# Kernel optimization log

Measured on AMD Instinct MI355X. Metric: run time of the kernel, lower is better.

Reference implementation:

```python
import jax, jax.numpy as jnp
import numpy as np

B, S, D = 4, 2048, 1024
H, DK, DV = 16, 64, 64

def setup_inputs() -> dict:
    key = jax.random.key(0)
    ks = jax.random.split(key, 14)
    sc = 0.02
    return {
        "q": jax.random.normal(ks[0], (B, S, D), jnp.float32),
        "k": jax.random.normal(ks[1], (B, S, D), jnp.float32),
        "v": jax.random.normal(ks[2], (B, S, D), jnp.float32),
        "Wq": jax.random.normal(ks[3], (D, H * DK), jnp.float32) * sc,
        "bq": jnp.zeros((H * DK,), jnp.float32),
        "Wk": jax.random.normal(ks[4], (D, H * DK), jnp.float32) * sc,
        "bk": jnp.zeros((H * DK,), jnp.float32),
        "Wv": jax.random.normal(ks[5], (D, H * DV), jnp.float32) * sc,
        "bv": jnp.zeros((H * DV,), jnp.float32),
        "Wo": jax.random.normal(ks[6], (H * DV, D), jnp.float32) * sc,
        "bo": jnp.zeros((D,), jnp.float32),
        "gamma": jnp.ones((D,), jnp.float32),
        "beta": jnp.zeros((D,), jnp.float32),
    }

def _layer_norm(x, gamma, beta, eps=1e-5):
    mu = jnp.mean(x, axis=-1, keepdims=True)
    var = jnp.mean(jnp.square(x - mu), axis=-1, keepdims=True)
    return (x - mu) * jax.lax.rsqrt(var + eps) * gamma + beta

def reference(q, k, v, Wq, bq, Wk, bk, Wv, bv, Wo, bo, gamma, beta):
    b, lq, _ = q.shape
    lk = k.shape[1]
    # projections -> [b, h, len, d]
    Q = (q @ Wq + bq).reshape(b, lq, H, DK).transpose(0, 2, 1, 3)
    K = (k @ Wk + bk).reshape(b, lk, H, DK).transpose(0, 2, 1, 3)
    V = (v @ Wv + bv).reshape(b, lk, H, DV).transpose(0, 2, 1, 3)
    scores = jnp.einsum("bhqd,bhkd->bhqk", Q, K) / np.sqrt(DK).astype(np.float32)
    attn = jax.nn.softmax(scores, axis=-1)
    out = jnp.einsum("bhqk,bhkd->bhqd", attn, V)
    out = out.transpose(0, 2, 1, 3).reshape(b, lq, H * DV)
    out = out @ Wo + bo
    # dropout is identity in eval mode
    out = _layer_norm(out + q, gamma, beta)
    return (out, attn)
```

## Files before the change

### kernel.cpp

```cpp
#include <hip/hip_runtime.h>
#include <stdint.h>

typedef unsigned short u16;
typedef unsigned int   u32;
typedef __attribute__((ext_vector_type(8))) short bf16x8;
typedef __attribute__((ext_vector_type(4))) float f32x4;
typedef __attribute__((ext_vector_type(4))) u32   u32x4;
typedef __attribute__((ext_vector_type(2))) u32   u32x2;

#define BB 4
#define SS 2048
#define DD 1024
#define HH 16
#define QSCALE 0.18033688011112042f

__device__ __forceinline__ u16 f2b(float f){
  u32 u = __builtin_bit_cast(u32, f);
  u32 r = (u + 0x7FFFu + ((u >> 16) & 1u)) >> 16;
  return (u16)r;
}
__device__ __forceinline__ float b2f(u16 h){
  return __builtin_bit_cast(float, (u32)h << 16);
}
__device__ __forceinline__ u32 cvtpk(float lo, float hi){
  u32 r; asm("v_cvt_pk_bf16_f32 %0, %1, %2" : "=v"(r) : "v"(lo), "v"(hi)); return r;
}

__device__ __forceinline__ void gload16(const u16* g, u16* l){
  __builtin_amdgcn_global_load_lds(
      (const __attribute__((address_space(1))) void*)(uintptr_t)g,
      (__attribute__((address_space(3))) void*)(uintptr_t)l,
      16, 0, 0);
}

__global__ __launch_bounds__(256)
void cvt_bf16_3(const float* __restrict__ q, const float* __restrict__ k,
                const float* __restrict__ v, u16* __restrict__ qo,
                u16* __restrict__ ko, u16* __restrict__ vo, int npack)
{
  const float* in = blockIdx.y == 0 ? q : (blockIdx.y == 1 ? k : v);
  u16* out        = blockIdx.y == 0 ? qo : (blockIdx.y == 1 ? ko : vo);
  for(int i = blockIdx.x * 256 + threadIdx.x; i < npack; i += gridDim.x * 256){
    const float4* p = (const float4*)in + 2 * (size_t)i;
    float4 a = p[0], b = p[1];
    u32x4 o;
    o.x = f2b(a.x) | ((u32)f2b(a.y) << 16);
    o.y = f2b(a.z) | ((u32)f2b(a.w) << 16);
    o.z = f2b(b.x) | ((u32)f2b(b.y) << 16);
    o.w = f2b(b.z) | ((u32)f2b(b.w) << 16);
    ((u32x4*)out)[i] = o;
  }
}

__global__ __launch_bounds__(256)
void transpose_cvt4(const float* __restrict__ W0, const float* __restrict__ W1,
                    const float* __restrict__ W2, const float* __restrict__ W3,
                    u16* __restrict__ T0, u16* __restrict__ T1,
                    u16* __restrict__ T2, u16* __restrict__ T3)
{
  const float* W = blockIdx.z == 0 ? W0 : (blockIdx.z == 1 ? W1 : (blockIdx.z == 2 ? W2 : W3));
  u16*        Wt = blockIdx.z == 0 ? T0 : (blockIdx.z == 1 ? T1 : (blockIdx.z == 2 ? T2 : T3));
  __shared__ float tile[64][65];
  const int tid = threadIdx.x;
  const int n0 = blockIdx.x * 64, k0 = blockIdx.y * 64;
  const int lr = tid >> 4, lc = tid & 15;
  #pragma unroll
  for(int i = 0; i < 4; ++i){
    float4 v = *(const float4*)(W + (size_t)(k0 + lr + 16*i) * DD + n0 + lc * 4);
    tile[lr + 16*i][lc*4 + 0] = v.x;
    tile[lr + 16*i][lc*4 + 1] = v.y;
    tile[lr + 16*i][lc*4 + 2] = v.z;
    tile[lr + 16*i][lc*4 + 3] = v.w;
  }
  __syncthreads();
  #pragma unroll
  for(int j = 0; j < 2; ++j){
    int idx = j * 256 + tid;
    int row = idx >> 3, seg = idx & 7;
    u32x4 o;
    o.x = f2b(tile[seg*8+0][row]) | ((u32)f2b(tile[seg*8+1][row]) << 16);
    o.y = f2b(tile[seg*8+2][row]) | ((u32)f2b(tile[seg*8+3][row]) << 16);
    o.z = f2b(tile[seg*8+4][row]) | ((u32)f2b(tile[seg*8+5][row]) << 16);
    o.w = f2b(tile[seg*8+6][row]) | ((u32)f2b(tile[seg*8+7][row]) << 16);
    *(u32x4*)(Wt + (size_t)(n0 + row) * DD + k0 + seg * 8) = o;
  }
}

__global__ __launch_bounds__(256)
void gemm_qkv(const u16* __restrict__ qA, const u16* __restrict__ kA, const u16* __restrict__ vA,
              const u16* __restrict__ BtQ, const u16* __restrict__ BtK, const u16* __restrict__ BtV,
              const float* __restrict__ bq, const float* __restrict__ bk, const float* __restrict__ bv,
              u16* __restrict__ Qo, u16* __restrict__ Ko, u16* __restrict__ Vo)
{
  const int mode = blockIdx.z;
  const u16* A   = mode == 0 ? qA  : (mode == 1 ? kA  : vA);
  const u16* Bt  = mode == 0 ? BtQ : (mode == 1 ? BtK : BtV);
  const float* bias = mode == 0 ? bq : (mode == 1 ? bk : bv);
  u16* Cout      = mode == 0 ? Qo  : (mode == 1 ? Ko  : Vo);

  __shared__ __align__(16) u16 smem[16384];
  u16* As = smem;
  u16* Bs = smem + 128*32;
  const int tid = threadIdx.x;
  const int w = tid >> 6, ln = tid & 63, g = ln >> 4, c16 = ln & 15;
  const int m0 = blockIdx.y * 128, n0 = blockIdx.x * 128;
  const int wr = (w >> 1) * 64, wc = (w & 1) * 64;

  f32x4 acc[4][4] = {};

  for(int kt = 0; kt < 1024; kt += 32){
    __syncthreads();
    {
      const int f0 = w * 2;
      #pragma unroll
      for(int j = 0; j < 2; ++j){
        int e = ((f0 + j) * 64 + ln) * 8;
        gload16(Bt + (size_t)(n0 + (e >> 5)) * 1024 + kt + (e & 31),
                Bs + (size_t)(f0 + j) * 512);
        gload16(A + (size_t)(m0 + (e >> 5)) * 1024 + kt + (e & 31),
                As + (size_t)(f0 + j) * 512);
      }
    }
    __syncthreads();
    bf16x8 a[4], b[4];
    #pragma unroll
    for(int mi = 0; mi < 4; ++mi)
      a[mi] = *(const bf16x8*)(As + (wr + mi*16 + c16) * 32 + g * 8);
    #pragma unroll
    for(int ni = 0; ni < 4; ++ni)
      b[ni] = *(const bf16x8*)(Bs + (wc + ni*16 + c16) * 32 + g * 8);
    #pragma unroll
    for(int mi = 0; mi < 4; ++mi)
      #pragma unroll
      for(int ni = 0; ni < 4; ++ni)
        acc[mi][ni] = __builtin_amdgcn_mfma_f32_16x16x32_bf16(a[mi], b[ni], acc[mi][ni], 0, 0, 0);
  }
  __syncthreads();

  char* st = (char*)smem + w * 8192;
  const float sc = (mode == 0) ? QSCALE : 1.f;
  const int bb = m0 >> 11;
  const int h  = (n0 + wc) >> 6;
  const int sbase = (m0 + wr) & 2047;

  if(mode < 2){
    #pragma unroll
    for(int ni = 0; ni < 4; ++ni){
      const float bvv = bias[n0 + wc + ni*16 + c16];
      const int gr = ni*2 + (c16 >> 3);
      const int within = (c16 & 7) * 2;
      #pragma unroll
      for(int mi = 0; mi < 4; ++mi)
        #pragma unroll
        for(int e = 0; e < 4; ++e){
          const int row = mi*16 + g*4 + e;
          *(u16*)(st + row*128 + ((gr ^ (row & 7)) << 4) + within)
              = f2b((acc[mi][ni][e] + bvv) * sc);
        }
    }
    asm volatile("s_waitcnt lgkmcnt(0)" ::: "memory");
    const int r8 = ln >> 3, jl = ln & 7;
    #pragma unroll
    for(int ii = 0; ii < 8; ++ii){
      const int row = ii*8 + r8;
      u16* dst = Cout + (((size_t)(bb*HH + h) * SS) + sbase + row) * 64 + jl*8;
      *(u32x4*)dst = *(const u32x4*)(st + row*128 + ((jl ^ (row & 7)) << 4));
    }
  } else {
    #pragma unroll
    for(int ni = 0; ni < 4; ++ni){
      const float bvv = bias[n0 + wc + ni*16 + c16];
      const int row = ni*16 + c16;
      #pragma unroll
      for(int mi = 0; mi < 4; ++mi)
        #pragma unroll
        for(int e = 0; e < 4; ++e){
          const int sl = mi*16 + g*4 + e;
          const int gr = sl >> 3;
          *(u16*)(st + row*128 + ((gr ^ (row & 7)) << 4) + (sl & 7) * 2)
              = f2b(acc[mi][ni][e] + bvv);
        }
    }
    asm volatile("s_waitcnt lgkmcnt(0)" ::: "memory");
    const int r8 = ln >> 3, jl = ln & 7;
    #pragma unroll
    for(int ii = 0; ii < 8; ++ii){
      const int d = ii*8 + r8;
      u16* dst = Cout + ((size_t)(bb*HH + h) * 64 + (n0 + wc - ((n0+wc)>>6<<6)) + d) * SS + sbase + jl*8;
      *(u32x4*)dst = *(const u32x4*)(st + d*128 + ((jl ^ (d & 7)) << 4));
    }
  }
}

__global__ __launch_bounds__(256)
void gemm_o(const u16* __restrict__ A, const u16* __restrict__ Bt,
            const float* __restrict__ bias, u16* __restrict__ Cout)
{
  __shared__ __align__(16) u16 smem[16384];
  u16* As = smem;
  u16* Bs = smem + 128*32;
  const int tid = threadIdx.x;
  const int w = tid >> 6, ln = tid & 63, g = ln >> 4, c16 = ln & 15;
  const int m0 = blockIdx.y * 128, n0 = blockIdx.x * 128;
  const int wr = (w >> 1) * 64, wc = (w & 1) * 64;

  f32x4 acc[4][4] = {};

  for(int kt = 0; kt < 1024; kt += 32){
    __syncthreads();
    {
      const int f0 = w * 2;
      #pragma unroll
      for(int j = 0; j < 2; ++j){
        int e = ((f0 + j) * 64 + ln) * 8;
        gload16(Bt + (size_t)(n0 + (e >> 5)) * 1024 + kt + (e & 31),
                Bs + (size_t)(f0 + j) * 512);
        gload16(A + (size_t)(m0 + (e >> 5)) * 1024 + kt + (e & 31),
                As + (size_t)(f0 + j) * 512);
      }
    }
    __syncthreads();
    bf16x8 a[4], b[4];
    #pragma unroll
    for(int mi = 0; mi < 4; ++mi)
      a[mi] = *(const bf16x8*)(As + (wr + mi*16 + c16) * 32 + g * 8);
    #pragma unroll
    for(int ni = 0; ni < 4; ++ni)
      b[ni] = *(const bf16x8*)(Bs + (wc + ni*16 + c16) * 32 + g * 8);
    #pragma unroll
    for(int mi = 0; mi < 4; ++mi)
      #pragma unroll
      for(int ni = 0; ni < 4; ++ni)
        acc[mi][ni] = __builtin_amdgcn_mfma_f32_16x16x32_bf16(a[mi], b[ni], acc[mi][ni], 0, 0, 0);
  }
  __syncthreads();

  char* st = (char*)smem + w * 8192;
  #pragma unroll
  for(int ni = 0; ni < 4; ++ni){
    const float bvv = bias[n0 + wc + ni*16 + c16];
    const int gr = ni*2 + (c16 >> 3);
    const int within = (c16 & 7) * 2;
    #pragma unroll
    for(int mi = 0; mi < 4; ++mi)
      #pragma unroll
      for(int e = 0; e < 4; ++e){
        const int row = mi*16 + g*4 + e;
        *(u16*)(st + row*128 + ((gr ^ (row & 7)) << 4) + within)
            = f2b(acc[mi][ni][e] + bvv);
      }
  }
  asm volatile("s_waitcnt lgkmcnt(0)" ::: "memory");
  const int r8 = ln >> 3, jl = ln & 7;
  #pragma unroll
  for(int ii = 0; ii < 8; ++ii){
    const int row = ii*8 + r8;
    u16* dst = Cout + (size_t)(m0 + wr + row) * 1024 + n0 + wc + jl*8;
    *(u32x4*)dst = *(const u32x4*)(st + row*128 + ((jl ^ (row & 7)) << 4));
  }
}

__global__ __launch_bounds__(256)
void attn8(const u16* __restrict__ Qb, const u16* __restrict__ Kb,
           const u16* __restrict__ Vt, float* __restrict__ attn_out,
           u16* __restrict__ AO)
{
  __shared__ __align__(16) u16 shm[32768];
  const int tid = threadIdx.x, w = tid >> 6, ln = tid & 63, g = ln >> 4, c = ln & 15;
  const int bh = blockIdx.y;
  const int q0 = blockIdx.x * 128 + w * 32;

  const u16* Qp = Qb + ((size_t)bh * SS + q0) * 64;
  const u16* Kp = Kb + (size_t)bh * SS * 64;
  const u16* Vp = Vt + (size_t)bh * 64 * SS;

  const bf16x8 bq00 = *(const bf16x8*)(Qp + c * 64 + g * 8);
  const bf16x8 bq01 = *(const bf16x8*)(Qp + c * 64 + 32 + g * 8);
  const bf16x8 bq10 = *(const bf16x8*)(Qp + (16 + c) * 64 + g * 8);
  const bf16x8 bq11 = *(const bf16x8*)(Qp + (16 + c) * 64 + 32 + g * 8);

  auto stageK = [&](int slot, int t){
    const u16* src = Kp + (size_t)t * 64 * 64;
    #pragma unroll
    for(int j = 0; j < 2; ++j){
      int idx = j * 256 + tid;
      int r = idx >> 3, s5 = idx & 7;
      gload16(src + r * 64 + (((s5 ^ (r & 7))) << 3), shm + slot * 4096 + (idx << 3));
    }
  };
  auto stageV = [&](int slot, int t){
    #pragma unroll
    for(int j = 0; j < 2; ++j){
      int idx = j * 256 + tid;
      int r = idx >> 3, s5 = idx & 7;
      gload16(Vp + (size_t)r * SS + t * 64 + (((s5 ^ (r & 7))) << 3),
              shm + 12288 + slot * 4096 + (idx << 3));
    }
  };

  float l0 = 0.f, l1 = 0.f;
  auto comp1 = [&](const u16* kb_){
    f32x4 s[2][4] = {};
    #pragma unroll
    for(int ch = 0; ch < 4; ++ch){
      const int r = ch * 16 + c;
      bf16x8 ka0 = *(const bf16x8*)(kb_ + r * 64 + ((g       ^ (c & 7)) << 3));
      bf16x8 ka1 = *(const bf16x8*)(kb_ + r * 64 + (((4 + g) ^ (c & 7)) << 3));
      s[0][ch] = __builtin_amdgcn_mfma_f32_16x16x32_bf16(ka0, bq00, s[0][ch], 0, 0, 0);
      s[0][ch] = __builtin_amdgcn_mfma_f32_16x16x32_bf16(ka1, bq01, s[0][ch], 0, 0, 0);
      s[1][ch] = __builtin_amdgcn_mfma_f32_16x16x32_bf16(ka0, bq10, s[1][ch], 0, 0, 0);
      s[1][ch] = __builtin_amdgcn_mfma_f32_16x16x32_bf16(ka1, bq11, s[1][ch], 0, 0, 0);
    }
    #pragma unroll
    for(int ch = 0; ch < 4; ++ch)
      #pragma unroll
      for(int e = 0; e < 4; ++e){
        l0 += __builtin_amdgcn_exp2f(s[0][ch][e]);
        l1 += __builtin_amdgcn_exp2f(s[1][ch][e]);
      }
  };

  stageK(0, 0); stageK(1, 1);
  asm volatile("s_waitcnt vmcnt(2)" ::: "memory");
  __builtin_amdgcn_s_barrier();
  for(int t = 0; t < 32; t += 2){
    if(t < 30){ stageK((t + 2) & 3, t + 2); stageK((t + 3) & 3, t + 3); }
    __builtin_amdgcn_sched_barrier(0);
    comp1(shm + (t & 3) * 4096);
    if(t < 30) asm volatile("s_waitcnt vmcnt(4)" ::: "memory");
    else       asm volatile("s_waitcnt vmcnt(0)" ::: "memory");
    __builtin_amdgcn_sched_barrier(0);
    comp1(shm + ((t + 1) & 3) * 4096);
    if(t < 30) asm volatile("s_waitcnt vmcnt(2)" ::: "memory");
    __builtin_amdgcn_s_barrier();
  }
  l0 += __shfl_xor(l0, 16, 64); l0 += __shfl_xor(l0, 32, 64);
  l1 += __shfl_xor(l1, 16, 64); l1 += __shfl_xor(l1, 32, 64);
  const float rl0 = 1.f / l0, rl1 = 1.f / l1;

  f32x4 acc[2][4] = {};
  float* aout = attn_out + ((size_t)bh * SS + q0) * SS;
  u16* pw0 = shm + 24576 + w * 2048;
  u16* pw1 = pw0 + 1024;

  stageK(0, 0); stageV(0, 0); stageK(1, 1); stageV(1, 1);
  asm volatile("s_waitcnt vmcnt(4)" ::: "memory");
  __builtin_amdgcn_s_barrier();

  for(int t = 0; t < 32; ++t){
    if(t < 30){ stageK((t + 2) % 3, t + 2); stageV((t + 2) % 3, t + 2); }
    __builtin_amdgcn_sched_barrier(0);
    const int kv0 = t * 64;
    const u16* kb_ = shm + (t % 3) * 4096;
    const u16* vb_ = shm + 12288 + (t % 3) * 4096;

    f32x4 s[2][4] = {};
    __builtin_amdgcn_s_setprio(1);
    #pragma unroll
    for(int ch = 0; ch < 4; ++ch){
      const int r = ch * 16 + c;
      bf16x8 ka0 = *(const bf16x8*)(kb_ + r * 64 + ((g       ^ (c & 7)) << 3));
      bf16x8 ka1 = *(const bf16x8*)(kb_ + r * 64 + (((4 + g) ^ (c & 7)) << 3));
      s[0][ch] = __builtin_amdgcn_mfma_f32_16x16x32_bf16(ka0, bq00, s[0][ch], 0, 0, 0);
      s[0][ch] = __builtin_amdgcn_mfma_f32_16x16x32_bf16(ka1, bq01, s[0][ch], 0, 0, 0);
      s[1][ch] = __builtin_amdgcn_mfma_f32_16x16x32_bf16(ka0, bq10, s[1][ch], 0, 0, 0);
      s[1][ch] = __builtin_amdgcn_mfma_f32_16x16x32_bf16(ka1, bq11, s[1][ch], 0, 0, 0);
    }
    __builtin_amdgcn_s_setprio(0);

    #pragma unroll
    for(int qb = 0; qb < 2; ++qb){
      const float rl = qb ? rl1 : rl0;
      u16* pw = qb ? pw1 : pw0;
      #pragma unroll
      for(int ch = 0; ch < 4; ++ch){
        float p0 = __builtin_amdgcn_exp2f(s[qb][ch][0]) * rl;
        float p1 = __builtin_amdgcn_exp2f(s[qb][ch][1]) * rl;
        float p2 = __builtin_amdgcn_exp2f(s[qb][ch][2]) * rl;
        float p3 = __builtin_amdgcn_exp2f(s[qb][ch][3]) * rl;
        u32x2 pk2 = { cvtpk(p0, p1), cvtpk(p2, p3) };
        *(u32x2*)((char*)pw + c * 128 + (((ch * 2 + (g >> 1)) ^ (c & 7)) << 4) + ((g & 1) << 3)) = pk2;
      }
    }
    asm volatile("s_waitcnt lgkmcnt(0)" ::: "memory");
    __builtin_amdgcn_sched_barrier(0);

    __builtin_amdgcn_s_setprio(1);
    #pragma unroll
    for(int kc = 0; kc < 2; ++kc){
      bf16x8 ap0 = *(const bf16x8*)((const char*)pw0 + c * 128 + (((kc * 4 + g) ^ (c & 7)) << 4));
      bf16x8 ap1 = *(const bf16x8*)((const char*)pw1 + c * 128 + (((kc * 4 + g) ^ (c & 7)) << 4));
      #pragma unroll
      for(int ni = 0; ni < 4; ++ni){
        bf16x8 bv = *(const bf16x8*)(vb_ + (ni * 16 + c) * 64 + (((kc * 4 + g) ^ (c & 7)) << 3));
        acc[0][ni] = __builtin_amdgcn_mfma_f32_16x16x32_bf16(ap0, bv, acc[0][ni], 0, 0, 0);
        acc[1][ni] = __builtin_amdgcn_mfma_f32_16x16x32_bf16(ap1, bv, acc[1][ni], 0, 0, 0);
      }
    }
    __builtin_amdgcn_s_setprio(0);

    {
      const int r8 = ln >> 3;
      const int jl = ln & 7;
      #pragma unroll
      for(int qb = 0; qb < 2; ++qb){
        const u16* pw = qb ? pw1 : pw0;
        #pragma unroll
        for(int rh = 0; rh < 2; ++rh){
          const int r = rh * 8 + r8;
          #pragma unroll
          for(int chf = 0; chf < 2; ++chf){
            const int jg = chf * 8 + jl;
            const int ch2 = jg >> 2, g2 = jg & 3;
            const int slot = ch2 * 2 + (g2 >> 1);
            u32x2 pk = *(const u32x2*)((const char*)pw + r * 128 +
                         (((slot ^ (r & 7))) << 4) + ((g2 & 1) << 3));
            f32x4 o;
            o[0] = b2f((u16)(pk.x & 0xFFFFu)); o[1] = b2f((u16)(pk.x >> 16));
            o[2] = b2f((u16)(pk.y & 0xFFFFu)); o[3] = b2f((u16)(pk.y >> 16));
            *(f32x4*)(aout + (size_t)(qb * 16 + r) * SS + kv0 + jg * 4) = o;
          }
        }
      }
    }

    if(t == 0)       asm volatile("s_waitcnt vmcnt(12)" ::: "memory");
    else if(t < 30)  asm volatile("s_waitcnt vmcnt(20)" ::: "memory");
    else if(t == 30) asm volatile("s_waitcnt vmcnt(16)" ::: "memory");
    __builtin_amdgcn_s_barrier();
  }

  u16* aos = pw0;
  #pragma unroll
  for(int qb = 0; qb < 2; ++qb)
    #pragma unroll
    for(int ni = 0; ni < 4; ++ni)
      #pragma unroll
      for(int e = 0; e < 4; ++e)
        aos[(qb * 16 + 4 * g + e) * 64 + ni * 16 + c] = f2b(acc[qb][ni][e]);
  asm volatile("s_waitcnt lgkmcnt(0)" ::: "memory");
  __builtin_amdgcn_sched_barrier(0);
  {
    const int bb = bh >> 4, h = bh & 15;
    #pragma unroll
    for(int p2 = 0; p2 < 4; ++p2){
      int idx = p2 * 64 + ln;
      int row = idx >> 3, col16 = (idx & 7) * 8;
      u16* dst = AO + ((size_t)bb * SS + q0 + row) * 1024 + h * 64 + col16;
      *(u32x4*)dst = *(const u32x4*)(aos + row * 64 + col16);
    }
  }
}

__global__ __launch_bounds__(256)
void ln_kernel(const u16* __restrict__ tmpb, const float* __restrict__ qin,
               const float* __restrict__ gamma, const float* __restrict__ beta,
               float* __restrict__ out)
{
  __shared__ float rs[4], rs2[4];
  const int row = blockIdx.x, tid = threadIdx.x;
  const int w = tid >> 6, ln = tid & 63;
  const uint2 tv = *(const uint2*)(tmpb + (size_t)row * 1024 + tid * 4);
  const float4 q4 = *(const float4*)(qin + (size_t)row * 1024 + tid * 4);
  const float xs0 = b2f((u16)(tv.x & 0xFFFFu)) + q4.x;
  const float xs1 = b2f((u16)(tv.x >> 16))     + q4.y;
  const float xs2 = b2f((u16)(tv.y & 0xFFFFu)) + q4.z;
  const float xs3 = b2f((u16)(tv.y >> 16))     + q4.w;
  float s  = xs0 + xs1 + xs2 + xs3;
  float s2 = xs0*xs0 + xs1*xs1 + xs2*xs2 + xs3*xs3;
  #pragma unroll
  for(int m = 1; m < 64; m <<= 1){
    s  += __shfl_xor(s,  m, 64);
    s2 += __shfl_xor(s2, m, 64);
  }
  if(ln == 0){ rs[w] = s; rs2[w] = s2; }
  __syncthreads();
  s  = rs[0]  + rs[1]  + rs[2]  + rs[3];
  s2 = rs2[0] + rs2[1] + rs2[2] + rs2[3];
  const float mu   = s * (1.f / 1024.f);
  const float var  = s2 * (1.f / 1024.f) - mu * mu;
  const float rstd = rsqrtf(var + 1e-5f);
  const float4 g4 = *(const float4*)(gamma + tid * 4);
  const float4 b4 = *(const float4*)(beta + tid * 4);
  float4 o;
  o.x = (xs0 - mu) * rstd * g4.x + b4.x;
  o.y = (xs1 - mu) * rstd * g4.y + b4.y;
  o.z = (xs2 - mu) * rstd * g4.z + b4.z;
  o.w = (xs3 - mu) * rstd * g4.w + b4.w;
  *(float4*)(out + (size_t)row * 1024 + tid * 4) = o;
}

extern "C" void kernel_launch(void* const* d_in, const int* in_sizes, int n_in,
                              void* d_out, int out_size, void* d_ws, size_t ws_size,
                              hipStream_t stream)
{
  (void)in_sizes; (void)n_in; (void)out_size; (void)ws_size;
  const float* q     = (const float*)d_in[0];
  const float* k     = (const float*)d_in[1];
  const float* v     = (const float*)d_in[2];
  const float* Wq    = (const float*)d_in[3];
  const float* bq    = (const float*)d_in[4];
  const float* Wk    = (const float*)d_in[5];
  const float* bk    = (const float*)d_in[6];
  const float* Wv    = (const float*)d_in[7];
  const float* bv    = (const float*)d_in[8];
  const float* Wo    = (const float*)d_in[9];
  const float* bo    = (const float*)d_in[10];
  const float* gamma = (const float*)d_in[11];
  const float* beta  = (const float*)d_in[12];

  char* p = (char*)d_ws;
  auto alloc = [&](size_t bytes) -> void* {
    void* r = (void*)p; p += (bytes + 255) & ~(size_t)255; return r;
  };
  const size_t NTOK = (size_t)BB * SS;
  u16* WtQ  = (u16*)alloc((size_t)DD * DD * 2);
  u16* WtK  = (u16*)alloc((size_t)DD * DD * 2);
  u16* WtV  = (u16*)alloc((size_t)DD * DD * 2);
  u16* WtO  = (u16*)alloc((size_t)DD * DD * 2);
  u16* Qb   = (u16*)alloc(NTOK * DD * 2);
  u16* Kb   = (u16*)alloc(NTOK * DD * 2);
  u16* Vtb  = (u16*)alloc(NTOK * DD * 2);
  u16* AO   = (u16*)alloc(NTOK * DD * 2);
  u16* qbf  = (u16*)alloc(NTOK * DD * 2);
  u16* kbf  = (u16*)alloc(NTOK * DD * 2);
  u16* vbf  = (u16*)alloc(NTOK * DD * 2);
  u16* tmpb = (u16*)alloc(NTOK * DD * 2);

  float* out0 = (float*)d_out;
  float* attn = out0 + NTOK * DD;

  const int NPACK = (int)(NTOK * DD / 8);
  cvt_bf16_3<<<dim3(1024, 3), 256, 0, stream>>>(q, k, v, qbf, kbf, vbf, NPACK);

  transpose_cvt4<<<dim3(16, 16, 4), 256, 0, stream>>>(
      Wq, Wk, Wv, Wo, WtQ, WtK, WtV, WtO);

  gemm_qkv<<<dim3(8, 64, 3), 256, 0, stream>>>(
      qbf, kbf, vbf, WtQ, WtK, WtV, bq, bk, bv, Qb, Kb, Vtb);

  attn8<<<dim3(16, 64), 256, 0, stream>>>(Qb, Kb, Vtb, attn, AO);

  gemm_o<<<dim3(8, 64), 256, 0, stream>>>(AO, WtO, bo, tmpb);
  ln_kernel<<<dim3(8192), 256, 0, stream>>>(tmpb, q, gamma, beta, out0);
}
```

Before: 461.6 us.

## Process two query tiles per block, fusing tile B's row-sum pass into tile A's output pass

Each attention block now handles two 128-row query groups. The softmax denominator pass for the second group is folded into the probability/PV pass of the first group, so K is streamed three times per two groups instead of four. The grid is also reordered so blockIdx.x indexes batch-head. This cuts K reloads and the separate sum pass for half the work, at the cost of fewer blocks (512 vs 1024), more registers for the extra Q fragments, and longer serial work per block.

```diff
diff --git a/kernel.cpp b/kernel.cpp
--- a/kernel.cpp
+++ b/kernel.cpp
@@ -260,24 +260,43 @@
   }
 }
 
+#define QKT(KB, Q00, Q01, Q10, Q11, S) do{                                             \
+  _Pragma("unroll")                                                                    \
+  for(int ch_ = 0; ch_ < 4; ++ch_){                                                    \
+    const int r_ = ch_ * 16 + c;                                                       \
+    bf16x8 ka0_ = *(const bf16x8*)((KB) + r_ * 64 + ((g       ^ (c & 7)) << 3));       \
+    bf16x8 ka1_ = *(const bf16x8*)((KB) + r_ * 64 + (((4 + g) ^ (c & 7)) << 3));       \
+    S[0][ch_] = __builtin_amdgcn_mfma_f32_16x16x32_bf16(ka0_, Q00, S[0][ch_], 0,0,0);  \
+    S[0][ch_] = __builtin_amdgcn_mfma_f32_16x16x32_bf16(ka1_, Q01, S[0][ch_], 0,0,0);  \
+    S[1][ch_] = __builtin_amdgcn_mfma_f32_16x16x32_bf16(ka0_, Q10, S[1][ch_], 0,0,0);  \
+    S[1][ch_] = __builtin_amdgcn_mfma_f32_16x16x32_bf16(ka1_, Q11, S[1][ch_], 0,0,0);  \
+  }                                                                                    \
+}while(0)
+
 __global__ __launch_bounds__(256)
-void attn8(const u16* __restrict__ Qb, const u16* __restrict__ Kb,
+void attn9(const u16* __restrict__ Qb, const u16* __restrict__ Kb,
            const u16* __restrict__ Vt, float* __restrict__ attn_out,
            u16* __restrict__ AO)
 {
   __shared__ __align__(16) u16 shm[32768];
   const int tid = threadIdx.x, w = tid >> 6, ln = tid & 63, g = ln >> 4, c = ln & 15;
-  const int bh = blockIdx.y;
-  const int q0 = blockIdx.x * 128 + w * 32;
-
-  const u16* Qp = Qb + ((size_t)bh * SS + q0) * 64;
-  const u16* Kp = Kb + (size_t)bh * SS * 64;
-  const u16* Vp = Vt + (size_t)bh * 64 * SS;
-
-  const bf16x8 bq00 = *(const bf16x8*)(Qp + c * 64 + g * 8);
-  const bf16x8 bq01 = *(const bf16x8*)(Qp + c * 64 + 32 + g * 8);
-  const bf16x8 bq10 = *(const bf16x8*)(Qp + (16 + c) * 64 + g * 8);
-  const bf16x8 bq11 = *(const bf16x8*)(Qp + (16 + c) * 64 + 32 + g * 8);
+  const int bh = blockIdx.x;
+  const int q0A = blockIdx.y * 256 + w * 32;
+  const int q0B = q0A + 128;
+
+  const u16* QpA = Qb + ((size_t)bh * SS + q0A) * 64;
+  const u16* QpB = Qb + ((size_t)bh * SS + q0B) * 64;
+  const u16* Kp  = Kb + (size_t)bh * SS * 64;
+  const u16* Vp  = Vt + (size_t)bh * 64 * SS;
+
+  const bf16x8 qA00 = *(const bf16x8*)(QpA + c * 64 + g * 8);
+  const bf16x8 qA01 = *(const bf16x8*)(QpA + c * 64 + 32 + g * 8);
+  const bf16x8 qA10 = *(const bf16x8*)(QpA + (16 + c) * 64 + g * 8);
+  const bf16x8 qA11 = *(const bf16x8*)(QpA + (16 + c) * 64 + 32 + g * 8);
+  const bf16x8 qB00 = *(const bf16x8*)(QpB + c * 64 + g * 8);
+  const bf16x8 qB01 = *(const bf16x8*)(QpB + c * 64 + 32 + g * 8);
+  const bf16x8 qB10 = *(const bf16x8*)(QpB + (16 + c) * 64 + g * 8);
+  const bf16x8 qB11 = *(const bf16x8*)(QpB + (16 + c) * 64 + 32 + g * 8);
 
   auto stageK = [&](int slot, int t){
     const u16* src = Kp + (size_t)t * 64 * 64;
@@ -298,75 +317,32 @@
     }
   };
 
-  float l0 = 0.f, l1 = 0.f;
-  auto comp1 = [&](const u16* kb_){
-    f32x4 s[2][4] = {};
-    #pragma unroll
-    for(int ch = 0; ch < 4; ++ch){
-      const int r = ch * 16 + c;
-      bf16x8 ka0 = *(const bf16x8*)(kb_ + r * 64 + ((g       ^ (c & 7)) << 3));
-      bf16x8 ka1 = *(const bf16x8*)(kb_ + r * 64 + (((4 + g) ^ (c & 7)) << 3));
-      s[0][ch] = __builtin_amdgcn_mfma_f32_16x16x32_bf16(ka0, bq00, s[0][ch], 0, 0, 0);
-      s[0][ch] = __builtin_amdgcn_mfma_f32_16x16x32_bf16(ka1, bq01, s[0][ch], 0, 0, 0);
-      s[1][ch] = __builtin_amdgcn_mfma_f32_16x16x32_bf16(ka0, bq10, s[1][ch], 0, 0, 0);
-      s[1][ch] = __builtin_amdgcn_mfma_f32_16x16x32_bf16(ka1, bq11, s[1][ch], 0, 0, 0);
-    }
-    #pragma unroll
-    for(int ch = 0; ch < 4; ++ch)
-      #pragma unroll
-      for(int e = 0; e < 4; ++e){
-        l0 += __builtin_amdgcn_exp2f(s[0][ch][e]);
-        l1 += __builtin_amdgcn_exp2f(s[1][ch][e]);
-      }
-  };
-
-  stageK(0, 0); stageK(1, 1);
-  asm volatile("s_waitcnt vmcnt(2)" ::: "memory");
-  __builtin_amdgcn_s_barrier();
-  for(int t = 0; t < 32; t += 2){
-    if(t < 30){ stageK((t + 2) & 3, t + 2); stageK((t + 3) & 3, t + 3); }
-    __builtin_amdgcn_sched_barrier(0);
-    comp1(shm + (t & 3) * 4096);
-    if(t < 30) asm volatile("s_waitcnt vmcnt(4)" ::: "memory");
-    else       asm volatile("s_waitcnt vmcnt(0)" ::: "memory");
-    __builtin_amdgcn_sched_barrier(0);
-    comp1(shm + ((t + 1) & 3) * 4096);
-    if(t < 30) asm volatile("s_waitcnt vmcnt(2)" ::: "memory");
-    __builtin_amdgcn_s_barrier();
-  }
-  l0 += __shfl_xor(l0, 16, 64); l0 += __shfl_xor(l0, 32, 64);
-  l1 += __shfl_xor(l1, 16, 64); l1 += __shfl_xor(l1, 32, 64);
-  const float rl0 = 1.f / l0, rl1 = 1.f / l1;
-
-  f32x4 acc[2][4] = {};
-  float* aout = attn_out + ((size_t)bh * SS + q0) * SS;
   u16* pw0 = shm + 24576 + w * 2048;
   u16* pw1 = pw0 + 1024;
 
-  stageK(0, 0); stageV(0, 0); stageK(1, 1); stageV(1, 1);
-  asm volatile("s_waitcnt vmcnt(4)" ::: "memory");
-  __builtin_amdgcn_s_barrier();
-
-  for(int t = 0; t < 32; ++t){
-    if(t < 30){ stageK((t + 2) % 3, t + 2); stageV((t + 2) % 3, t + 2); }
-    __builtin_amdgcn_sched_barrier(0);
+  auto p2_tile = [&](int t, const u16* kb_, const u16* vb_,
+                     const bf16x8& Q00, const bf16x8& Q01, const bf16x8& Q10, const bf16x8& Q11,
+                     float rl0, float rl1, f32x4 (&acc)[2][4], float* aout, bool withB,
+                     float& lB0, float& lB1){
     const int kv0 = t * 64;
-    const u16* kb_ = shm + (t % 3) * 4096;
-    const u16* vb_ = shm + 12288 + (t % 3) * 4096;
-
     f32x4 s[2][4] = {};
     __builtin_amdgcn_s_setprio(1);
-    #pragma unroll
-    for(int ch = 0; ch < 4; ++ch){
-      const int r = ch * 16 + c;
-      bf16x8 ka0 = *(const bf16x8*)(kb_ + r * 64 + ((g       ^ (c & 7)) << 3));
-      bf16x8 ka1 = *(const bf16x8*)(kb_ + r * 64 + (((4 + g) ^ (c & 7)) << 3));
-      s[0][ch] = __builtin_amdgcn_mfma_f32_16x16x32_bf16(ka0, bq00, s[0][ch], 0, 0, 0);
-      s[0][ch] = __builtin_amdgcn_mfma_f32_16x16x32_bf16(ka1, bq01, s[0][ch], 0, 0, 0);
-      s[1][ch] = __builtin_amdgcn_mfma_f32_16x16x32_bf16(ka0, bq10, s[1][ch], 0, 0, 0);
-      s[1][ch] = __builtin_amdgcn_mfma_f32_16x16x32_bf16(ka1, bq11, s[1][ch], 0, 0, 0);
-    }
+    QKT(kb_, Q00, Q01, Q10, Q11, s);
     __builtin_amdgcn_s_setprio(0);
+
+    if(withB){
+      f32x4 sb[2][4] = {};
+      __builtin_amdgcn_s_setprio(1);
+      QKT(kb_, qB00, qB01, qB10, qB11, sb);
+      __builtin_amdgcn_s_setprio(0);
+      #pragma unroll
+      for(int ch = 0; ch < 4; ++ch)
+        #pragma unroll
+        for(int e = 0; e < 4; ++e){
+          lB0 += __builtin_amdgcn_exp2f(sb[0][ch][e]);
+          lB1 += __builtin_amdgcn_exp2f(sb[1][ch][e]);
+        }
+    }
 
     #pragma unroll
     for(int qb = 0; qb < 2; ++qb){
@@ -428,19 +404,19 @@
     else if(t < 30)  asm volatile("s_waitcnt vmcnt(20)" ::: "memory");
     else if(t == 30) asm volatile("s_waitcnt vmcnt(16)" ::: "memory");
     __builtin_amdgcn_s_barrier();
-  }
-
-  u16* aos = pw0;
-  #pragma unroll
-  for(int qb = 0; qb < 2; ++qb)
-    #pragma unroll
-    for(int ni = 0; ni < 4; ++ni)
-      #pragma unroll
-      for(int e = 0; e < 4; ++e)
-        aos[(qb * 16 + 4 * g + e) * 64 + ni * 16 + c] = f2b(acc[qb][ni][e]);
-  asm volatile("s_waitcnt lgkmcnt(0)" ::: "memory");
-  __builtin_amdgcn_sched_barrier(0);
-  {
+  };
+
+  auto ao_epilogue = [&](f32x4 (&acc)[2][4], int q0){
+    u16* aos = pw0;
+    #pragma unroll
+    for(int qb = 0; qb < 2; ++qb)
+      #pragma unroll
+      for(int ni = 0; ni < 4; ++ni)
+        #pragma unroll
+        for(int e = 0; e < 4; ++e)
+          aos[(qb * 16 + 4 * g + e) * 64 + ni * 16 + c] = f2b(acc[qb][ni][e]);
+    asm volatile("s_waitcnt lgkmcnt(0)" ::: "memory");
+    __builtin_amdgcn_sched_barrier(0);
     const int bb = bh >> 4, h = bh & 15;
     #pragma unroll
     for(int p2 = 0; p2 < 4; ++p2){
@@ -449,7 +425,72 @@
       u16* dst = AO + ((size_t)bb * SS + q0 + row) * 1024 + h * 64 + col16;
       *(u32x4*)dst = *(const u32x4*)(aos + row * 64 + col16);
     }
-  }
+  };
+
+  float l0 = 0.f, l1 = 0.f;
+  auto comp1 = [&](const u16* kb_){
+    f32x4 s[2][4] = {};
+    QKT(kb_, qA00, qA01, qA10, qA11, s);
+    #pragma unroll
+    for(int ch = 0; ch < 4; ++ch)
+      #pragma unroll
+      for(int e = 0; e < 4; ++e){
+        l0 += __builtin_amdgcn_exp2f(s[0][ch][e]);
+        l1 += __builtin_amdgcn_exp2f(s[1][ch][e]);
+      }
+  };
+
+  stageK(0, 0); stageK(1, 1);
+  asm volatile("s_waitcnt vmcnt(2)" ::: "memory");
+  __builtin_amdgcn_s_barrier();
+  for(int t = 0; t < 32; t += 2){
+    if(t < 30){ stageK((t + 2) & 3, t + 2); stageK((t + 3) & 3, t + 3); }
+    __builtin_amdgcn_sched_barrier(0);
+    comp1(shm + (t & 3) * 4096);
+    if(t < 30) asm volatile("s_waitcnt vmcnt(4)" ::: "memory");
+    else       asm volatile("s_waitcnt vmcnt(0)" ::: "memory");
+    __builtin_amdgcn_sched_barrier(0);
+    comp1(shm + ((t + 1) & 3) * 4096);
+    if(t < 30) asm volatile("s_waitcnt vmcnt(2)" ::: "memory");
+    __builtin_amdgcn_s_barrier();
+  }
+  l0 += __shfl_xor(l0, 16, 64); l0 += __shfl_xor(l0, 32, 64);
+  l1 += __shfl_xor(l1, 16, 64); l1 += __shfl_xor(l1, 32, 64);
+  const float rlA0 = 1.f / l0, rlA1 = 1.f / l1;
+
+  f32x4 accA[2][4] = {};
+  float lB0 = 0.f, lB1 = 0.f;
+  float* aoutA = attn_out + ((size_t)bh * SS + q0A) * SS;
+
+  stageK(0, 0); stageV(0, 0); stageK(1, 1); stageV(1, 1);
+  asm volatile("s_waitcnt vmcnt(4)" ::: "memory");
+  __builtin_amdgcn_s_barrier();
+  for(int t = 0; t < 32; ++t){
+    if(t < 30){ stageK((t + 2) % 3, t + 2); stageV((t + 2) % 3, t + 2); }
+    __builtin_amdgcn_sched_barrier(0);
+    p2_tile(t, shm + (t % 3) * 4096, shm + 12288 + (t % 3) * 4096,
+            qA00, qA01, qA10, qA11, rlA0, rlA1, accA, aoutA, true, lB0, lB1);
+  }
+  ao_epilogue(accA, q0A);
+
+  lB0 += __shfl_xor(lB0, 16, 64); lB0 += __shfl_xor(lB0, 32, 64);
+  lB1 += __shfl_xor(lB1, 16, 64); lB1 += __shfl_xor(lB1, 32, 64);
+  const float rlB0 = 1.f / lB0, rlB1 = 1.f / lB1;
+
+  f32x4 accB[2][4] = {};
+  float dum0, dum1;
+  float* aoutB = attn_out + ((size_t)bh * SS + q0B) * SS;
+
+  stageK(0, 0); stageV(0, 0); stageK(1, 1); stageV(1, 1);
+  asm volatile("s_waitcnt vmcnt(4)" ::: "memory");
+  __builtin_amdgcn_s_barrier();
+  for(int t = 0; t < 32; ++t){
+    if(t < 30){ stageK((t + 2) % 3, t + 2); stageV((t + 2) % 3, t + 2); }
+    __builtin_amdgcn_sched_barrier(0);
+    p2_tile(t, shm + (t % 3) * 4096, shm + 12288 + (t % 3) * 4096,
+            qB00, qB01, qB10, qB11, rlB0, rlB1, accB, aoutB, false, dum0, dum1);
+  }
+  ao_epilogue(accB, q0B);
 }
 
 __global__ __launch_bounds__(256)
@@ -539,7 +580,7 @@
   gemm_qkv<<<dim3(8, 64, 3), 256, 0, stream>>>(
       qbf, kbf, vbf, WtQ, WtK, WtV, bq, bk, bv, Qb, Kb, Vtb);
 
-  attn8<<<dim3(16, 64), 256, 0, stream>>>(Qb, Kb, Vtb, attn, AO);
+  attn9<<<dim3(64, 8), 256, 0, stream>>>(Qb, Kb, Vtb, attn, AO);
 
   gemm_o<<<dim3(8, 64), 256, 0, stream>>>(AO, WtO, bo, tmpb);
   ln_kernel<<<dim3(8192), 256, 0, stream>>>(tmpb, q, gamma, beta, out0);
```

After: 536.7 us. +16.3%, slower.

## Double GEMM K-tile to 64 with XOR-swizzled LDS; one-wave-per-row LayerNorm

Applied to the files above, without the earlier changes.

The shared GEMM main loop now stages a K-step of 64 instead of 32. Global loads are placed into LDS with an XOR swizzle so the MFMA operand reads avoid bank conflicts. This halves the number of barrier-separated iterations in the QKV and output projections while keeping the same LDS footprint. The LayerNorm kernel now gives each wave a full row with a shuffle-only reduction, removing the shared-memory reduction and block barrier, at the cost of more registers per thread.

```diff
diff --git a/kernel.cpp b/kernel.cpp
--- a/kernel.cpp
+++ b/kernel.cpp
@@ -86,6 +86,48 @@
   }
 }
 
+#define GEMM_CORE(A_, Bt_)                                                             \
+  f32x4 acc[4][4] = {};                                                                \
+  for(int kt = 0; kt < 1024; kt += 64){                                                \
+    __syncthreads();                                                                   \
+    {                                                                                  \
+      const int f0 = w * 4;                                                            \
+      _Pragma("unroll")                                                                \
+      for(int j = 0; j < 4; ++j){                                                      \
+        int idx = (f0 + j) * 64 + ln;                                                  \
+        int row = idx >> 3, s5 = idx & 7;                                              \
+        int gcol = (s5 ^ (row & 7)) * 8;                                               \
+        gload16(Bt_ + (size_t)(n0 + row) * 1024 + kt + gcol, Bs + (size_t)(f0+j)*512); \
+        gload16(A_  + (size_t)(m0 + row) * 1024 + kt + gcol, As + (size_t)(f0+j)*512); \
+      }                                                                                \
+    }                                                                                  \
+    __syncthreads();                                                                   \
+    bf16x8 a0[4], a1[4], b0[4], b1[4];                                                 \
+    _Pragma("unroll")                                                                  \
+    for(int mi = 0; mi < 4; ++mi){                                                     \
+      const int r = wr + mi*16 + c16;                                                  \
+      a0[mi] = *(const bf16x8*)(As + r * 64 + ((g       ^ (r & 7)) << 3));             \
+      a1[mi] = *(const bf16x8*)(As + r * 64 + (((4 + g) ^ (r & 7)) << 3));             \
+    }                                                                                  \
+    _Pragma("unroll")                                                                  \
+    for(int ni = 0; ni < 4; ++ni){                                                     \
+      const int r = wc + ni*16 + c16;                                                  \
+      b0[ni] = *(const bf16x8*)(Bs + r * 64 + ((g       ^ (r & 7)) << 3));             \
+      b1[ni] = *(const bf16x8*)(Bs + r * 64 + (((4 + g) ^ (r & 7)) << 3));             \
+    }                                                                                  \
+    _Pragma("unroll")                                                                  \
+    for(int mi = 0; mi < 4; ++mi)                                                      \
+      _Pragma("unroll")                                                                \
+      for(int ni = 0; ni < 4; ++ni)                                                    \
+        acc[mi][ni] = __builtin_amdgcn_mfma_f32_16x16x32_bf16(a0[mi], b0[ni], acc[mi][ni], 0, 0, 0); \
+    _Pragma("unroll")                                                                  \
+    for(int mi = 0; mi < 4; ++mi)                                                      \
+      _Pragma("unroll")                                                                \
+      for(int ni = 0; ni < 4; ++ni)                                                    \
+        acc[mi][ni] = __builtin_amdgcn_mfma_f32_16x16x32_bf16(a1[mi], b1[ni], acc[mi][ni], 0, 0, 0); \
+  }                                                                                    \
+  __syncthreads();
+
 __global__ __launch_bounds__(256)
 void gemm_qkv(const u16* __restrict__ qA, const u16* __restrict__ kA, const u16* __restrict__ vA,
               const u16* __restrict__ BtQ, const u16* __restrict__ BtK, const u16* __restrict__ BtV,
@@ -100,42 +142,13 @@
 
   __shared__ __align__(16) u16 smem[16384];
   u16* As = smem;
-  u16* Bs = smem + 128*32;
+  u16* Bs = smem + 128*64;
   const int tid = threadIdx.x;
   const int w = tid >> 6, ln = tid & 63, g = ln >> 4, c16 = ln & 15;
   const int m0 = blockIdx.y * 128, n0 = blockIdx.x * 128;
   const int wr = (w >> 1) * 64, wc = (w & 1) * 64;
 
-  f32x4 acc[4][4] = {};
-
-  for(int kt = 0; kt < 1024; kt += 32){
-    __syncthreads();
-    {
-      const int f0 = w * 2;
-      #pragma unroll
-      for(int j = 0; j < 2; ++j){
-        int e = ((f0 + j) * 64 + ln) * 8;
-        gload16(Bt + (size_t)(n0 + (e >> 5)) * 1024 + kt + (e & 31),
-                Bs + (size_t)(f0 + j) * 512);
-        gload16(A + (size_t)(m0 + (e >> 5)) * 1024 + kt + (e & 31),
-                As + (size_t)(f0 + j) * 512);
-      }
-    }
-    __syncthreads();
-    bf16x8 a[4], b[4];
-    #pragma unroll
-    for(int mi = 0; mi < 4; ++mi)
-      a[mi] = *(const bf16x8*)(As + (wr + mi*16 + c16) * 32 + g * 8);
-    #pragma unroll
-    for(int ni = 0; ni < 4; ++ni)
-      b[ni] = *(const bf16x8*)(Bs + (wc + ni*16 + c16) * 32 + g * 8);
-    #pragma unroll
-    for(int mi = 0; mi < 4; ++mi)
-      #pragma unroll
-      for(int ni = 0; ni < 4; ++ni)
-        acc[mi][ni] = __builtin_amdgcn_mfma_f32_16x16x32_bf16(a[mi], b[ni], acc[mi][ni], 0, 0, 0);
-  }
-  __syncthreads();
+  GEMM_CORE(A, Bt)
 
   char* st = (char*)smem + w * 8192;
   const float sc = (mode == 0) ? QSCALE : 1.f;
@@ -198,42 +211,13 @@
 {
   __shared__ __align__(16) u16 smem[16384];
   u16* As = smem;
-  u16* Bs = smem + 128*32;
+  u16* Bs = smem + 128*64;
   const int tid = threadIdx.x;
   const int w = tid >> 6, ln = tid & 63, g = ln >> 4, c16 = ln & 15;
   const int m0 = blockIdx.y * 128, n0 = blockIdx.x * 128;
   const int wr = (w >> 1) * 64, wc = (w & 1) * 64;
 
-  f32x4 acc[4][4] = {};
-
-  for(int kt = 0; kt < 1024; kt += 32){
-    __syncthreads();
-    {
-      const int f0 = w * 2;
-      #pragma unroll
-      for(int j = 0; j < 2; ++j){
-        int e = ((f0 + j) * 64 + ln) * 8;
-        gload16(Bt + (size_t)(n0 + (e >> 5)) * 1024 + kt + (e & 31),
-                Bs + (size_t)(f0 + j) * 512);
-        gload16(A + (size_t)(m0 + (e >> 5)) * 1024 + kt + (e & 31),
-                As + (size_t)(f0 + j) * 512);
-      }
-    }
-    __syncthreads();
-    bf16x8 a[4], b[4];
-    #pragma unroll
-    for(int mi = 0; mi < 4; ++mi)
-      a[mi] = *(const bf16x8*)(As + (wr + mi*16 + c16) * 32 + g * 8);
-    #pragma unroll
-    for(int ni = 0; ni < 4; ++ni)
-      b[ni] = *(const bf16x8*)(Bs + (wc + ni*16 + c16) * 32 + g * 8);
-    #pragma unroll
-    for(int mi = 0; mi < 4; ++mi)
-      #pragma unroll
-      for(int ni = 0; ni < 4; ++ni)
-        acc[mi][ni] = __builtin_amdgcn_mfma_f32_16x16x32_bf16(a[mi], b[ni], acc[mi][ni], 0, 0, 0);
-  }
-  __syncthreads();
+  GEMM_CORE(A, Bt)
 
   char* st = (char*)smem + w * 8192;
   #pragma unroll
@@ -457,37 +441,45 @@
                const float* __restrict__ gamma, const float* __restrict__ beta,
                float* __restrict__ out)
 {
-  __shared__ float rs[4], rs2[4];
-  const int row = blockIdx.x, tid = threadIdx.x;
-  const int w = tid >> 6, ln = tid & 63;
-  const uint2 tv = *(const uint2*)(tmpb + (size_t)row * 1024 + tid * 4);
-  const float4 q4 = *(const float4*)(qin + (size_t)row * 1024 + tid * 4);
-  const float xs0 = b2f((u16)(tv.x & 0xFFFFu)) + q4.x;
-  const float xs1 = b2f((u16)(tv.x >> 16))     + q4.y;
-  const float xs2 = b2f((u16)(tv.y & 0xFFFFu)) + q4.z;
-  const float xs3 = b2f((u16)(tv.y >> 16))     + q4.w;
-  float s  = xs0 + xs1 + xs2 + xs3;
-  float s2 = xs0*xs0 + xs1*xs1 + xs2*xs2 + xs3*xs3;
+  const int tid = threadIdx.x, w = tid >> 6, ln = tid & 63;
+  const int row = blockIdx.x * 4 + w;
+  const u16*   tp = tmpb + (size_t)row * 1024;
+  const float* qp = qin  + (size_t)row * 1024;
+  float xs[16];
+  float s = 0.f, s2 = 0.f;
+  #pragma unroll
+  for(int ck = 0; ck < 4; ++ck){
+    const int col = ck * 256 + ln * 4;
+    const uint2 tv = *(const uint2*)(tp + col);
+    const float4 q4 = *(const float4*)(qp + col);
+    float x0 = b2f((u16)(tv.x & 0xFFFFu)) + q4.x;
+    float x1 = b2f((u16)(tv.x >> 16))     + q4.y;
+    float x2 = b2f((u16)(tv.y & 0xFFFFu)) + q4.z;
+    float x3 = b2f((u16)(tv.y >> 16))     + q4.w;
+    xs[ck*4+0] = x0; xs[ck*4+1] = x1; xs[ck*4+2] = x2; xs[ck*4+3] = x3;
+    s  += x0 + x1 + x2 + x3;
+    s2 += x0*x0 + x1*x1 + x2*x2 + x3*x3;
+  }
   #pragma unroll
   for(int m = 1; m < 64; m <<= 1){
     s  += __shfl_xor(s,  m, 64);
     s2 += __shfl_xor(s2, m, 64);
   }
-  if(ln == 0){ rs[w] = s; rs2[w] = s2; }
-  __syncthreads();
-  s  = rs[0]  + rs[1]  + rs[2]  + rs[3];
-  s2 = rs2[0] + rs2[1] + rs2[2] + rs2[3];
   const float mu   = s * (1.f / 1024.f);
   const float var  = s2 * (1.f / 1024.f) - mu * mu;
   const float rstd = rsqrtf(var + 1e-5f);
-  const float4 g4 = *(const float4*)(gamma + tid * 4);
-  const float4 b4 = *(const float4*)(beta + tid * 4);
-  float4 o;
-  o.x = (xs0 - mu) * rstd * g4.x + b4.x;
-  o.y = (xs1 - mu) * rstd * g4.y + b4.y;
-  o.z = (xs2 - mu) * rstd * g4.z + b4.z;
-  o.w = (xs3 - mu) * rstd * g4.w + b4.w;
-  *(float4*)(out + (size_t)row * 1024 + tid * 4) = o;
+  #pragma unroll
+  for(int ck = 0; ck < 4; ++ck){
+    const int col = ck * 256 + ln * 4;
+    const float4 g4 = *(const float4*)(gamma + col);
+    const float4 b4 = *(const float4*)(beta + col);
+    float4 o;
+    o.x = (xs[ck*4+0] - mu) * rstd * g4.x + b4.x;
+    o.y = (xs[ck*4+1] - mu) * rstd * g4.y + b4.y;
+    o.z = (xs[ck*4+2] - mu) * rstd * g4.z + b4.z;
+    o.w = (xs[ck*4+3] - mu) * rstd * g4.w + b4.w;
+    *(float4*)(out + (size_t)row * 1024 + col) = o;
+  }
 }
 
 extern "C" void kernel_launch(void* const* d_in, const int* in_sizes, int n_in,
@@ -542,5 +534,5 @@
   attn8<<<dim3(16, 64), 256, 0, stream>>>(Qb, Kb, Vtb, attn, AO);
 
   gemm_o<<<dim3(8, 64), 256, 0, stream>>>(AO, WtO, bo, tmpb);
-  ln_kernel<<<dim3(8192), 256, 0, stream>>>(tmpb, q, gamma, beta, out0);
-}
+  ln_kernel<<<dim3(2048), 256, 0, stream>>>(tmpb, q, gamma, beta, out0);
+}
```

Measured after the change: 453.9 us. About the same (-1.7%).
